# Optimization experiments

Measured on AMD Instinct MI355X. Metric: run time of the kernel, lower is better.

The kernel has to match this reference:

```python
import jax, jax.numpy as jnp
import numpy as np

N_NODES = 20000
N_EDGES = 256000
DIM = 128
N_LAYERS = 4


def _bn(x, gamma, beta, eps=1e-5):
    # BatchNorm1d in training mode: batch statistics over the node/edge axis
    mu = x.mean(0)
    var = ((x - mu) ** 2).mean(0)
    return gamma * (x - mu) * jax.lax.rsqrt(var + eps) + beta


def setup_inputs() -> dict:
    key = jax.random.key(0)
    ks = jax.random.split(key, 32)
    s = 1.0 / np.sqrt(DIM)
    inp = {
        'h': jax.random.normal(ks[0], (N_NODES, DIM), jnp.float32),
        'e': jax.random.normal(ks[1], (N_EDGES, DIM), jnp.float32),
        'src': jax.random.randint(ks[2], (N_EDGES,), 0, N_NODES, jnp.int32),
        'dst': jax.random.randint(ks[3], (N_EDGES,), 0, N_NODES, jnp.int32),
        'W_emb_h': jax.random.normal(ks[4], (DIM, DIM), jnp.float32) * s,
        'b_emb_h': jnp.zeros((DIM,), jnp.float32),
        'W_emb_e': jax.random.normal(ks[5], (DIM, DIM), jnp.float32) * s,
        'b_emb_e': jnp.zeros((DIM,), jnp.float32),
    }
    for i, nm in enumerate(['A', 'B', 'C', 'D', 'E']):
        inp[nm + 'w'] = jax.random.normal(ks[6 + i], (N_LAYERS, DIM, DIM), jnp.float32) * s
        inp[nm + 'b'] = jnp.zeros((N_LAYERS, DIM), jnp.float32)
    inp['gh'] = jnp.ones((N_LAYERS, DIM), jnp.float32)
    inp['bh'] = jnp.zeros((N_LAYERS, DIM), jnp.float32)
    inp['ge'] = jnp.ones((N_LAYERS, DIM), jnp.float32)
    inp['be'] = jnp.zeros((N_LAYERS, DIM), jnp.float32)
    return inp


def reference(h, e, src, dst, W_emb_h, b_emb_h, W_emb_e, b_emb_e,
              Aw, Ab, Bw, Bb, Cw, Cb, Dw, Db, Ew, Eb, gh, bh, ge, be):
    n_nodes = h.shape[0]
    # input embeddings
    h = h @ W_emb_h + b_emb_h
    e = e @ W_emb_e + b_emb_e
    for l in range(Aw.shape[0]):
        h_in, e_in = h, e
        Ah = h @ Aw[l] + Ab[l]
        Bh = h @ Bw[l] + Bb[l]
        Dh = h @ Dw[l] + Db[l]
        Eh = h @ Ew[l] + Eb[l]
        Ce = e @ Cw[l] + Cb[l]
        # edge gates: e_ij = D h_i + E h_j + C e_ij  (edge i->j)
        e_new = Dh[src] + Eh[dst] + Ce            # [E, D]
        sigma = jax.nn.sigmoid(e_new)
        num = jax.ops.segment_sum(sigma * Bh[src], dst, num_segments=n_nodes)
        den = jax.ops.segment_sum(sigma, dst, num_segments=n_nodes)
        h_new = Ah + num / (den + 1e-6)
        h_new = _bn(h_new, gh[l], bh[l])
        e_new = _bn(e_new, ge[l], be[l])
        # relu + residual (dropout = 0)
        h = h_in + jax.nn.relu(h_new)
        e = e_in + jax.nn.relu(e_new)
    return h
```

## Files before the change

kernel.cpp:

```cpp
#include <hip/hip_runtime.h>
#include <hip/hip_bf16.h>

typedef __attribute__((ext_vector_type(8))) short short8;
typedef __attribute__((ext_vector_type(4))) float floatx4;
typedef __attribute__((ext_vector_type(4))) unsigned short ushortx4;

typedef __attribute__((address_space(3))) unsigned int lds_u32;
typedef __attribute__((address_space(1))) const unsigned int g_u32;

__device__ __forceinline__ float bf2f(unsigned short u) {
    union { float f; unsigned int i; } v; v.i = ((unsigned int)u) << 16; return v.f;
}
__device__ __forceinline__ unsigned short f2bf(float f) {
    union { float f; unsigned int i; } v; v.f = f;
    unsigned int r = v.i + 0x7fffu + ((v.i >> 16) & 1u);
    return (unsigned short)(r >> 16);
}

__global__ void deg_count(const int* __restrict__ dst, int* __restrict__ deg, int E) {
    int i = blockIdx.x * 256 + threadIdx.x;
    if (i < E) atomicAdd(&deg[dst[i]], 1);
}

__global__ __launch_bounds__(1024) void scan_rowptr(const int* __restrict__ deg,
                                                    int* __restrict__ rowptr,
                                                    int* __restrict__ cursor, int N) {
    const int CH = 20;
    __shared__ int buf[1024];
    int t = threadIdx.x;
    int base = t * CH;
    int local[CH];
    int tot = 0;
#pragma unroll
    for (int k = 0; k < CH; ++k) {
        int i = base + k;
        int v = (i < N) ? deg[i] : 0;
        local[k] = tot;
        tot += v;
    }
    buf[t] = tot;
    __syncthreads();
    for (int off = 1; off < 1024; off <<= 1) {
        int x = (t >= off) ? buf[t - off] : 0;
        __syncthreads();
        buf[t] += x;
        __syncthreads();
    }
    int excl = buf[t] - tot;
#pragma unroll
    for (int k = 0; k < CH; ++k) {
        int i = base + k;
        if (i < N) { rowptr[i] = excl + local[k]; cursor[i] = excl + local[k]; }
    }
    if (t == 1023) rowptr[N] = buf[1023];
}

__global__ void scatter_edges(const int* __restrict__ src, const int* __restrict__ dst,
                              int* __restrict__ cursor, int* __restrict__ eix,
                              int* __restrict__ sx, int* __restrict__ dstx, int E) {
    int i = blockIdx.x * 256 + threadIdx.x;
    if (i >= E) return;
    int d = dst[i];
    int pos = atomicAdd(&cursor[d], 1);
    eix[pos] = i;
    sx[pos] = src[i];
    dstx[pos] = d;
}

__global__ void transpose_w(const float* __restrict__ Wh,
                            const float* __restrict__ We,
                            const float* __restrict__ Aw,
                            const float* __restrict__ Bw,
                            const float* __restrict__ Cw,
                            const float* __restrict__ Dw,
                            const float* __restrict__ Ew,
                            unsigned short* __restrict__ Wt) {
    int i = blockIdx.x * 256 + threadIdx.x;
    const int total = 22 * 16384;
    if (i >= total) return;
    int slot = i >> 14;
    int r = i & 16383;
    int n = r >> 7;
    int k = r & 127;
    const float* srcp;
    if (slot == 0) srcp = Wh;
    else if (slot == 1) srcp = We;
    else {
        int t = slot - 2;
        int l = t / 5, w = t % 5;
        const float* bases[5] = {Aw, Bw, Cw, Dw, Ew};
        srcp = bases[w] + l * 16384;
    }
    Wt[i] = f2bf(srcp[k * 128 + n]);
}

template <int IN_F32, int OUT_BF16, int GATHER>
__global__ __launch_bounds__(256) void gemm_lds(const void* __restrict__ Ain,
                                                const int* __restrict__ ridx,
                                                const unsigned short* __restrict__ Wt,
                                                const float* __restrict__ bias,
                                                void* __restrict__ Cout,
                                                int nTiles, int Mrows) {
    constexpr int ROWB = IN_F32 ? 512 : 256;
    constexpr int RSH = IN_F32 ? 9 : 8;
    constexpr int TILEB = 64 * ROWB;
    constexpr int PERW = TILEB / 4;
    constexpr int ROUNDS = PERW / 1024;
    __shared__ unsigned char smem[2][TILEB];

    const int lane = threadIdx.x & 63;
    const int wv = threadIdx.x >> 6;
    const int m16 = lane & 15;
    const int kg = lane >> 4;

    short8 b[4][2];
#pragma unroll
    for (int j = 0; j < 2; ++j)
#pragma unroll
        for (int ks = 0; ks < 4; ++ks)
            b[ks][j] = *(const short8*)(Wt + ((wv * 2 + j) * 16 + m16) * 128 + ks * 32 + kg * 8);
    floatx4 bv[2];
#pragma unroll
    for (int j = 0; j < 2; ++j)
        bv[j] = *(const floatx4*)(bias + (wv * 2 + j) * 16 + kg * 4);

    const unsigned char* Ab = (const unsigned char*)Ain;

    int t0 = blockIdx.x;
    if (t0 >= nTiles) return;

    auto stage = [&](int bufsel, int t) {
#pragma unroll
        for (int r = 0; r < ROUNDS; ++r) {
            int d = wv * PERW + r * 1024 + lane * 16;
            int row = d >> RSH;
            int scol;
            if (IN_F32)
                scol = (d ^ ((row & 3) << 5)) & (ROWB - 1);
            else
                scol = (d ^ ((row & 7) << 4)) & (ROWB - 1);
            int grow = t * 64 + row;
            grow = grow < Mrows ? grow : Mrows - 1;
            if (GATHER) grow = ridx[grow];
            const unsigned char* gp = Ab + (size_t)grow * ROWB + scol;
            unsigned char* lp = &smem[bufsel][wv * PERW + r * 1024];
            __builtin_amdgcn_global_load_lds((g_u32*)gp, (lds_u32*)lp, 16, 0, 0);
        }
    };

    int cur = 0;
    stage(0, t0);
    __syncthreads();

    for (int t = t0; t < nTiles; t += gridDim.x) {
        int tn = t + gridDim.x;
        if (tn < nTiles) stage(cur ^ 1, tn);

        const unsigned char* sb = smem[cur];
#pragma unroll
        for (int st = 0; st < 4; ++st) {
            short8 a[4];
#pragma unroll
            for (int ks = 0; ks < 4; ++ks) {
                if (IN_F32) {
                    int aoff = (st * 16 + m16) * 512 + ks * 128 + kg * 32;
                    aoff ^= (m16 & 3) << 5;
                    floatx4 f0 = *(const floatx4*)(sb + aoff);
                    floatx4 f1 = *(const floatx4*)(sb + aoff + 16);
                    short8 tt;
                    tt[0] = (short)f2bf(f0[0]); tt[1] = (short)f2bf(f0[1]);
                    tt[2] = (short)f2bf(f0[2]); tt[3] = (short)f2bf(f0[3]);
                    tt[4] = (short)f2bf(f1[0]); tt[5] = (short)f2bf(f1[1]);
                    tt[6] = (short)f2bf(f1[2]); tt[7] = (short)f2bf(f1[3]);
                    a[ks] = tt;
                } else {
                    int aoff = (st * 16 + m16) * 256 + ks * 64 + kg * 16;
                    aoff ^= (m16 & 7) << 4;
                    a[ks] = *(const short8*)(sb + aoff);
                }
            }
            floatx4 acc0 = (floatx4){0.f, 0.f, 0.f, 0.f};
            floatx4 acc1 = (floatx4){0.f, 0.f, 0.f, 0.f};
#pragma unroll
            for (int ks = 0; ks < 4; ++ks) {
                acc0 = __builtin_amdgcn_mfma_f32_16x16x32_bf16(b[ks][0], a[ks], acc0, 0, 0, 0);
                acc1 = __builtin_amdgcn_mfma_f32_16x16x32_bf16(b[ks][1], a[ks], acc1, 0, 0, 0);
            }
            size_t row = (size_t)t * 64 + st * 16 + m16;
#pragma unroll
            for (int j = 0; j < 2; ++j) {
                int c0 = (wv * 2 + j) * 16 + kg * 4;
                floatx4 accj = j ? acc1 : acc0;
                if (OUT_BF16) {
                    ushortx4 o;
#pragma unroll
                    for (int i = 0; i < 4; ++i) o[i] = f2bf(accj[i] + bv[j][i]);
                    *(ushortx4*)((unsigned short*)Cout + row * 128 + c0) = o;
                } else {
                    floatx4 o;
#pragma unroll
                    for (int i = 0; i < 4; ++i) o[i] = accj[i] + bv[j][i];
                    *(floatx4*)((float*)Cout + row * 128 + c0) = o;
                }
            }
        }
        __syncthreads();
        cur ^= 1;
    }
}

template <int STATS>
__global__ __launch_bounds__(256) void gemm_ce(const unsigned short* __restrict__ Ain,
                                               const unsigned short* __restrict__ Wt,
                                               const float* __restrict__ bias,
                                               const int* __restrict__ sx,
                                               const int* __restrict__ dstx,
                                               const unsigned short* __restrict__ Dh16,
                                               const unsigned short* __restrict__ Eh16,
                                               unsigned short* __restrict__ e_new,
                                               float* __restrict__ sums,
                                               int nTiles) {
    constexpr int TILEB = 64 * 256;
    constexpr int PERW = TILEB / 4;
    constexpr int ROUNDS = PERW / 1024;
    __shared__ unsigned char smem[2][TILEB];
    __shared__ float ls[256];

    const int lane = threadIdx.x & 63;
    const int wv = threadIdx.x >> 6;
    const int m16 = lane & 15;
    const int kg = lane >> 4;

    short8 b[4][2];
#pragma unroll
    for (int j = 0; j < 2; ++j)
#pragma unroll
        for (int ks = 0; ks < 4; ++ks)
            b[ks][j] = *(const short8*)(Wt + ((wv * 2 + j) * 16 + m16) * 128 + ks * 32 + kg * 8);
    floatx4 bv[2];
#pragma unroll
    for (int j = 0; j < 2; ++j)
        bv[j] = *(const floatx4*)(bias + (wv * 2 + j) * 16 + kg * 4);

    float es[2][4], eq[2][4];
#pragma unroll
    for (int j = 0; j < 2; ++j)
#pragma unroll
        for (int i = 0; i < 4; ++i) { es[j][i] = 0.f; eq[j][i] = 0.f; }

    const unsigned char* Ab = (const unsigned char*)Ain;

    int t0 = blockIdx.x;

    auto stage = [&](int bufsel, int t) {
#pragma unroll
        for (int r = 0; r < ROUNDS; ++r) {
            int d = wv * PERW + r * 1024 + lane * 16;
            int row = d >> 8;
            int scol = (d ^ ((row & 7) << 4)) & 255;
            const unsigned char* gp = Ab + (size_t)(t * 64 + row) * 256 + scol;
            unsigned char* lp = &smem[bufsel][wv * PERW + r * 1024];
            __builtin_amdgcn_global_load_lds((g_u32*)gp, (lds_u32*)lp, 16, 0, 0);
        }
    };

    int cur = 0;
    if (t0 < nTiles) {
        stage(0, t0);
        __syncthreads();

        for (int t = t0; t < nTiles; t += gridDim.x) {
            int tn = t + gridDim.x;
            if (tn < nTiles) stage(cur ^ 1, tn);

            const unsigned char* sb = smem[cur];
#pragma unroll
            for (int st = 0; st < 4; ++st) {
                int erow = t * 64 + st * 16 + m16;
                int sr = sx[erow];
                int dr = dstx[erow];
                short8 a[4];
#pragma unroll
                for (int ks = 0; ks < 4; ++ks) {
                    int aoff = (st * 16 + m16) * 256 + ks * 64 + kg * 16;
                    aoff ^= (m16 & 7) << 4;
                    a[ks] = *(const short8*)(sb + aoff);
                }
                floatx4 acc0 = (floatx4){0.f, 0.f, 0.f, 0.f};
                floatx4 acc1 = (floatx4){0.f, 0.f, 0.f, 0.f};
#pragma unroll
                for (int ks = 0; ks < 4; ++ks) {
                    acc0 = __builtin_amdgcn_mfma_f32_16x16x32_bf16(b[ks][0], a[ks], acc0, 0, 0, 0);
                    acc1 = __builtin_amdgcn_mfma_f32_16x16x32_bf16(b[ks][1], a[ks], acc1, 0, 0, 0);
                }
#pragma unroll
                for (int j = 0; j < 2; ++j) {
                    int c0 = (wv * 2 + j) * 16 + kg * 4;
                    floatx4 accj = j ? acc1 : acc0;
                    ushortx4 dh = *(const ushortx4*)(Dh16 + (size_t)sr * 128 + c0);
                    ushortx4 eh = *(const ushortx4*)(Eh16 + (size_t)dr * 128 + c0);
                    ushortx4 o;
#pragma unroll
                    for (int i = 0; i < 4; ++i) {
                        float en = accj[i] + bv[j][i] + bf2f(dh[i]) + bf2f(eh[i]);
                        o[i] = f2bf(en);
                        if (STATS) { es[j][i] += en; eq[j][i] += en * en; }
                    }
                    *(ushortx4*)(e_new + (size_t)erow * 128 + c0) = o;
                }
            }
            __syncthreads();
            cur ^= 1;
        }
    }

    if (STATS) {
        ls[threadIdx.x] = 0.f;
        __syncthreads();
#pragma unroll
        for (int j = 0; j < 2; ++j) {
            int c0 = (wv * 2 + j) * 16 + kg * 4;
#pragma unroll
            for (int i = 0; i < 4; ++i) {
                atomicAdd(&ls[c0 + i], es[j][i]);
                atomicAdd(&ls[(c0 + i) ^ 128], eq[j][i]);
            }
        }
        __syncthreads();
        atomicAdd(&sums[256 + threadIdx.x], ls[threadIdx.x]);
    }
}

__global__ __launch_bounds__(1024) void gemm_h4(const float* __restrict__ h_cur,
                                                const unsigned short* __restrict__ WtL,
                                                const float* __restrict__ Abi,
                                                const float* __restrict__ Bbi,
                                                const float* __restrict__ Dbi,
                                                const float* __restrict__ Ebi,
                                                float* __restrict__ AhB,
                                                unsigned short* __restrict__ Bh16,
                                                unsigned short* __restrict__ Dh16,
                                                unsigned short* __restrict__ Eh16,
                                                int nStrips) {
    const int lane = threadIdx.x & 63;
    const int w = threadIdx.x >> 6;
    const int grp = w >> 2;
    const int ntb = (w & 3) * 2;
    const int m16 = lane & 15;
    const int kg = lane >> 4;

    const int slotmap[4] = {0, 1, 3, 4};
    const float* biasmap[4] = {Abi, Bbi, Dbi, Ebi};
    const unsigned short* Wm = WtL + slotmap[grp] * 16384;
    const float* bp = biasmap[grp];

    short8 bf[4][2];
    floatx4 bv[2];
#pragma unroll
    for (int j = 0; j < 2; ++j) {
#pragma unroll
        for (int ks = 0; ks < 4; ++ks)
            bf[ks][j] = *(const short8*)(Wm + ((ntb + j) * 16 + m16) * 128 + ks * 32 + kg * 8);
        bv[j] = *(const floatx4*)(bp + (ntb + j) * 16 + kg * 4);
    }

    for (int s = blockIdx.x; s < nStrips; s += gridDim.x) {
        size_t rowBase = ((size_t)s * 16 + m16) * 128;
        short8 a[4];
#pragma unroll
        for (int ks = 0; ks < 4; ++ks) {
            int off = ks * 32 + kg * 8;
            floatx4 f0 = *(const floatx4*)(h_cur + rowBase + off);
            floatx4 f1 = *(const floatx4*)(h_cur + rowBase + off + 4);
            short8 t;
            t[0] = (short)f2bf(f0[0]); t[1] = (short)f2bf(f0[1]);
            t[2] = (short)f2bf(f0[2]); t[3] = (short)f2bf(f0[3]);
            t[4] = (short)f2bf(f1[0]); t[5] = (short)f2bf(f1[1]);
            t[6] = (short)f2bf(f1[2]); t[7] = (short)f2bf(f1[3]);
            a[ks] = t;
        }

        floatx4 acc0 = (floatx4){0.f, 0.f, 0.f, 0.f};
        floatx4 acc1 = (floatx4){0.f, 0.f, 0.f, 0.f};
#pragma unroll
        for (int ks = 0; ks < 4; ++ks) {
            acc0 = __builtin_amdgcn_mfma_f32_16x16x32_bf16(bf[ks][0], a[ks], acc0, 0, 0, 0);
            acc1 = __builtin_amdgcn_mfma_f32_16x16x32_bf16(bf[ks][1], a[ks], acc1, 0, 0, 0);
        }

        size_t r = (size_t)s * 16 + m16;
        if (grp == 0) {
            floatx4 o0, o1;
#pragma unroll
            for (int i = 0; i < 4; ++i) { o0[i] = acc0[i] + bv[0][i]; o1[i] = acc1[i] + bv[1][i]; }
            *(floatx4*)(AhB + r * 128 + (ntb + 0) * 16 + kg * 4) = o0;
            *(floatx4*)(AhB + r * 128 + (ntb + 1) * 16 + kg * 4) = o1;
        } else {
            unsigned short* outp = (grp == 1) ? Bh16 : (grp == 2) ? Dh16 : Eh16;
            ushortx4 o0, o1;
#pragma unroll
            for (int i = 0; i < 4; ++i) {
                o0[i] = f2bf(acc0[i] + bv[0][i]);
                o1[i] = f2bf(acc1[i] + bv[1][i]);
            }
            *(ushortx4*)(outp + r * 128 + (ntb + 0) * 16 + kg * 4) = o0;
            *(ushortx4*)(outp + r * 128 + (ntb + 1) * 16 + kg * 4) = o1;
        }
    }
}

__global__ __launch_bounds__(256) void node_aggregate(const unsigned short* __restrict__ e_new,
                                                      const unsigned short* __restrict__ Bh16,
                                                      const int* __restrict__ rowptr,
                                                      const int* __restrict__ sx,
                                                      const float* __restrict__ Ah,
                                                      float* __restrict__ h_new,
                                                      float* __restrict__ sums, int N) {
    const int q = threadIdx.x & 31;
    const int g = threadIdx.x >> 5;
    float hs[4] = {0.f, 0.f, 0.f, 0.f};
    float hq[4] = {0.f, 0.f, 0.f, 0.f};
    for (int d = blockIdx.x * 8 + g; d < N; d += gridDim.x * 8) {
        int beg = rowptr[d], end = rowptr[d + 1];
        float num[4] = {0.f, 0.f, 0.f, 0.f};
        float den[4] = {0.f, 0.f, 0.f, 0.f};
        int j = beg;
        for (; j + 3 < end; j += 4) {
            int s0 = sx[j], s1 = sx[j + 1], s2 = sx[j + 2], s3 = sx[j + 3];
            ushortx4 e0 = *(const ushortx4*)(e_new + (size_t)j * 128 + q * 4);
            ushortx4 e1 = *(const ushortx4*)(e_new + (size_t)(j + 1) * 128 + q * 4);
            ushortx4 e2 = *(const ushortx4*)(e_new + (size_t)(j + 2) * 128 + q * 4);
            ushortx4 e3 = *(const ushortx4*)(e_new + (size_t)(j + 3) * 128 + q * 4);
            ushortx4 b0 = *(const ushortx4*)(Bh16 + (size_t)s0 * 128 + q * 4);
            ushortx4 b1 = *(const ushortx4*)(Bh16 + (size_t)s1 * 128 + q * 4);
            ushortx4 b2 = *(const ushortx4*)(Bh16 + (size_t)s2 * 128 + q * 4);
            ushortx4 b3 = *(const ushortx4*)(Bh16 + (size_t)s3 * 128 + q * 4);
#pragma unroll
            for (int k = 0; k < 4; ++k) {
                float sg0 = __builtin_amdgcn_rcpf(1.f + __expf(-bf2f(e0[k])));
                float sg1 = __builtin_amdgcn_rcpf(1.f + __expf(-bf2f(e1[k])));
                float sg2 = __builtin_amdgcn_rcpf(1.f + __expf(-bf2f(e2[k])));
                float sg3 = __builtin_amdgcn_rcpf(1.f + __expf(-bf2f(e3[k])));
                den[k] += (sg0 + sg1) + (sg2 + sg3);
                num[k] += sg0 * bf2f(b0[k]) + sg1 * bf2f(b1[k])
                        + sg2 * bf2f(b2[k]) + sg3 * bf2f(b3[k]);
            }
        }
        for (; j < end; ++j) {
            int s0 = sx[j];
            ushortx4 e0 = *(const ushortx4*)(e_new + (size_t)j * 128 + q * 4);
            ushortx4 b0 = *(const ushortx4*)(Bh16 + (size_t)s0 * 128 + q * 4);
#pragma unroll
            for (int k = 0; k < 4; ++k) {
                float sg0 = __builtin_amdgcn_rcpf(1.f + __expf(-bf2f(e0[k])));
                den[k] += sg0;
                num[k] += sg0 * bf2f(b0[k]);
            }
        }
        floatx4 ah = *(const floatx4*)(Ah + (size_t)d * 128 + q * 4);
        floatx4 out;
#pragma unroll
        for (int k = 0; k < 4; ++k) {
            float v = ah[k] + num[k] / (den[k] + 1e-6f);
            out[k] = v;
            hs[k] += v;
            hq[k] += v * v;
        }
        *(floatx4*)(h_new + (size_t)d * 128 + q * 4) = out;
    }
    __shared__ float ls[256];
    ls[threadIdx.x] = 0.f;
    __syncthreads();
#pragma unroll
    for (int k = 0; k < 4; ++k) {
        atomicAdd(&ls[q * 4 + k], hs[k]);
        atomicAdd(&ls[128 + q * 4 + k], hq[k]);
    }
    __syncthreads();
    atomicAdd(&sums[threadIdx.x], ls[threadIdx.x]);
}

__global__ void finalize_stats(const float* __restrict__ sums,
                               const float* __restrict__ gh,
                               const float* __restrict__ bh,
                               const float* __restrict__ ge,
                               const float* __restrict__ be,
                               float* __restrict__ coef, int N, int E) {
    int c = threadIdx.x;
    if (c >= 128) return;
    float muh = sums[c] / (float)N;
    float vh = fmaxf(sums[128 + c] / (float)N - muh * muh, 0.f);
    float rsh = rsqrtf(vh + 1e-5f);
    float g = gh[c], bt = bh[c];
    coef[c] = g * rsh;
    coef[128 + c] = bt - g * rsh * muh;
    float mue = sums[256 + c] / (float)E;
    float ve = fmaxf(sums[384 + c] / (float)E - mue * mue, 0.f);
    float rse = rsqrtf(ve + 1e-5f);
    float g2 = ge[c], b2 = be[c];
    coef[256 + c] = g2 * rse;
    coef[384 + c] = b2 - g2 * rse * mue;
}

__global__ __launch_bounds__(256) void h_update(const float* __restrict__ h_new,
                                                const float* __restrict__ coef,
                                                float* __restrict__ h_cur,
                                                float* __restrict__ out, int N) {
    const int c = threadIdx.x & 127;
    float sa = coef[c], sb = coef[128 + c];
    int total = N * 128;
    for (int i = blockIdx.x * blockDim.x + threadIdx.x; i < total; i += gridDim.x * blockDim.x) {
        float v = h_new[i] * sa + sb;
        v = v > 0.f ? v : 0.f;
        float h = h_cur[i] + v;
        h_cur[i] = h;
        if (out) out[i] = h;
    }
}

__global__ __launch_bounds__(256) void e_update(const unsigned short* __restrict__ e_new,
                                                const float* __restrict__ coef,
                                                unsigned short* __restrict__ e_cur, int E) {
    int total8 = E * 16;
    for (int idx = blockIdx.x * blockDim.x + threadIdx.x; idx < total8;
         idx += gridDim.x * blockDim.x) {
        int c8 = (idx & 15) * 8;
        short8 en = *(const short8*)(e_new + (size_t)idx * 8);
        short8 ec = *(const short8*)(e_cur + (size_t)idx * 8);
        floatx4 sa0 = *(const floatx4*)(coef + 256 + c8);
        floatx4 sa1 = *(const floatx4*)(coef + 256 + c8 + 4);
        floatx4 sb0 = *(const floatx4*)(coef + 384 + c8);
        floatx4 sb1 = *(const floatx4*)(coef + 384 + c8 + 4);
        short8 r;
#pragma unroll
        for (int k = 0; k < 8; ++k) {
            float sa = (k < 4) ? sa0[k] : sa1[k - 4];
            float sb = (k < 4) ? sb0[k] : sb1[k - 4];
            float v = bf2f((unsigned short)en[k]) * sa + sb;
            v = v > 0.f ? v : 0.f;
            r[k] = (short)f2bf(bf2f((unsigned short)ec[k]) + v);
        }
        *(short8*)(e_cur + (size_t)idx * 8) = r;
    }
}

extern "C" void kernel_launch(void* const* d_in, const int* in_sizes, int n_in,
                              void* d_out, int out_size, void* d_ws, size_t ws_size,
                              hipStream_t stream) {
    const int N = 20000, E = 256000, L = 4;
    const int NPAD = 20032;

    const float* h_in = (const float*)d_in[0];
    const float* e_in = (const float*)d_in[1];
    const int* src = (const int*)d_in[2];
    const int* dst = (const int*)d_in[3];
    const float* Wemb_h = (const float*)d_in[4];
    const float* bemb_h = (const float*)d_in[5];
    const float* Wemb_e = (const float*)d_in[6];
    const float* bemb_e = (const float*)d_in[7];
    const float* Aw = (const float*)d_in[8];
    const float* Abi = (const float*)d_in[9];
    const float* Bw = (const float*)d_in[10];
    const float* Bbi = (const float*)d_in[11];
    const float* Cw = (const float*)d_in[12];
    const float* Cbi = (const float*)d_in[13];
    const float* Dw = (const float*)d_in[14];
    const float* Dbi = (const float*)d_in[15];
    const float* Ew = (const float*)d_in[16];
    const float* Ebi = (const float*)d_in[17];
    const float* gh = (const float*)d_in[18];
    const float* bh = (const float*)d_in[19];
    const float* ge = (const float*)d_in[20];
    const float* be = (const float*)d_in[21];

    char* p = (char*)d_ws;
    auto carve = [&](size_t bytes) {
        void* r = (void*)p;
        p += ((bytes + 255) & ~(size_t)255);
        return r;
    };
    unsigned short* Wt = (unsigned short*)carve((size_t)22 * 16384 * 2);
    float* h_cur = (float*)carve((size_t)NPAD * 128 * 4);
    unsigned short* e_cur = (unsigned short*)carve((size_t)E * 128 * 2);
    unsigned short* e_new = (unsigned short*)carve((size_t)E * 128 * 2);
    float* AhB = (float*)carve((size_t)N * 128 * 4);
    unsigned short* Bh16 = (unsigned short*)carve((size_t)N * 128 * 2);
    unsigned short* Dh16 = (unsigned short*)carve((size_t)N * 128 * 2);
    unsigned short* Eh16 = (unsigned short*)carve((size_t)N * 128 * 2);
    float* h_newB = (float*)carve((size_t)N * 128 * 4);
    float* sums = (float*)carve(4 * 128 * 4);
    float* coef = (float*)carve(4 * 128 * 4);
    int* deg = (int*)carve((size_t)N * 4);
    int* rowptr = (int*)carve((size_t)(N + 1) * 4);
    int* cursor = (int*)carve((size_t)N * 4);
    int* eix = (int*)carve((size_t)E * 4);
    int* sx = (int*)carve((size_t)E * 4);
    int* dstx = (int*)carve((size_t)E * 4);

    hipMemsetAsync(deg, 0, (size_t)N * 4, stream);
    deg_count<<<(E + 255) / 256, 256, 0, stream>>>(dst, deg, E);
    scan_rowptr<<<1, 1024, 0, stream>>>(deg, rowptr, cursor, N);
    scatter_edges<<<(E + 255) / 256, 256, 0, stream>>>(src, dst, cursor, eix, sx, dstx, E);

    transpose_w<<<(22 * 16384 + 255) / 256, 256, 0, stream>>>(Wemb_h, Wemb_e, Aw, Bw, Cw, Dw, Ew, Wt);

    gemm_lds<1, 0, 0><<<313, 256, 0, stream>>>(h_in, nullptr, Wt + 0 * 16384, bemb_h,
                                               h_cur, 313, N);
    gemm_lds<1, 1, 1><<<1024, 256, 0, stream>>>(e_in, eix, Wt + 1 * 16384, bemb_e,
                                                e_cur, E / 64, E);

    for (int l = 0; l < L; ++l) {
        int last = (l == L - 1);
        hipMemsetAsync(sums, 0, 4 * 128 * 4, stream);
        const unsigned short* WtL = Wt + (size_t)(2 + l * 5) * 16384;
        gemm_h4<<<250, 1024, 0, stream>>>(h_cur, WtL, Abi + l * 128, Bbi + l * 128,
                                          Dbi + l * 128, Ebi + l * 128, AhB, Bh16, Dh16, Eh16,
                                          N / 16);
        if (!last)
            gemm_ce<1><<<1024, 256, 0, stream>>>(e_cur, WtL + 2 * 16384, Cbi + l * 128,
                                                 sx, dstx, Dh16, Eh16, e_new, sums, E / 64);
        else
            gemm_ce<0><<<1024, 256, 0, stream>>>(e_cur, WtL + 2 * 16384, Cbi + l * 128,
                                                 sx, dstx, Dh16, Eh16, e_new, sums, E / 64);
        node_aggregate<<<1250, 256, 0, stream>>>(e_new, Bh16, rowptr, sx, AhB,
                                                 h_newB, sums, N);
        finalize_stats<<<1, 128, 0, stream>>>(sums, gh + l * 128, bh + l * 128, ge + l * 128,
                                              be + l * 128, coef, N, E);
        h_update<<<512, 256, 0, stream>>>(h_newB, coef, h_cur, last ? (float*)d_out : nullptr, N);
        if (!last) e_update<<<2048, 256, 0, stream>>>(e_new, coef, e_cur, E);
    }
}
```

Measured before the change: 1.046 ms.

## Fuse sigmoid-gated scatter aggregation into edge GEMM with segmented atomics

Computes the sigmoid gate and sigma*Bh products inside the edge GEMM epilogue. Runs of equal destinations within each 16-row strip are pre-reduced with a shuffle scan, and the sums go to per-node num/den buffers via global float atomics. The separate CSR aggregation pass, and in the last layer the e_new store, are removed; a light node_combine kernel does the division and stats. In exchange it adds a large per-layer memset, many global atomics (edges are dst-sorted, so runs shorten them), and nondeterministic summation order.

Measured after the change: 1.477 ms. 41.2% more time.

```diff
diff --git a/kernel.cpp b/kernel.cpp
--- a/kernel.cpp
+++ b/kernel.cpp
@@ -215,9 +215,12 @@
                                                const float* __restrict__ bias,
                                                const int* __restrict__ sx,
                                                const int* __restrict__ dstx,
+                                               const unsigned short* __restrict__ Bh16,
                                                const unsigned short* __restrict__ Dh16,
                                                const unsigned short* __restrict__ Eh16,
                                                unsigned short* __restrict__ e_new,
+                                               float* __restrict__ num,
+                                               float* __restrict__ den,
                                                float* __restrict__ sums,
                                                int nTiles) {
     constexpr int TILEB = 64 * 256;
@@ -273,12 +276,27 @@
             int tn = t + gridDim.x;
             if (tn < nTiles) stage(cur ^ 1, tn);
 
-            const unsigned char* sb = smem[cur];
+            int sxv[4], dxv[4];
 #pragma unroll
             for (int st = 0; st < 4; ++st) {
                 int erow = t * 64 + st * 16 + m16;
-                int sr = sx[erow];
-                int dr = dstx[erow];
+                sxv[st] = sx[erow];
+                dxv[st] = dstx[erow];
+            }
+
+            const unsigned char* sb = smem[cur];
+#pragma unroll
+            for (int st = 0; st < 4; ++st) {
+                int erow = t * 64 + st * 16 + m16;
+                int sr = sxv[st], dr = dxv[st];
+                ushortx4 dh[2], eh[2], bh[2];
+#pragma unroll
+                for (int j = 0; j < 2; ++j) {
+                    int c0 = (wv * 2 + j) * 16 + kg * 4;
+                    dh[j] = *(const ushortx4*)(Dh16 + (size_t)sr * 128 + c0);
+                    eh[j] = *(const ushortx4*)(Eh16 + (size_t)dr * 128 + c0);
+                    bh[j] = *(const ushortx4*)(Bh16 + (size_t)sr * 128 + c0);
+                }
                 short8 a[4];
 #pragma unroll
                 for (int ks = 0; ks < 4; ++ks) {
@@ -293,20 +311,48 @@
                     acc0 = __builtin_amdgcn_mfma_f32_16x16x32_bf16(b[ks][0], a[ks], acc0, 0, 0, 0);
                     acc1 = __builtin_amdgcn_mfma_f32_16x16x32_bf16(b[ks][1], a[ks], acc1, 0, 0, 0);
                 }
+                float nm[2][4], dn[2][4];
 #pragma unroll
                 for (int j = 0; j < 2; ++j) {
                     int c0 = (wv * 2 + j) * 16 + kg * 4;
                     floatx4 accj = j ? acc1 : acc0;
-                    ushortx4 dh = *(const ushortx4*)(Dh16 + (size_t)sr * 128 + c0);
-                    ushortx4 eh = *(const ushortx4*)(Eh16 + (size_t)dr * 128 + c0);
                     ushortx4 o;
 #pragma unroll
                     for (int i = 0; i < 4; ++i) {
-                        float en = accj[i] + bv[j][i] + bf2f(dh[i]) + bf2f(eh[i]);
-                        o[i] = f2bf(en);
-                        if (STATS) { es[j][i] += en; eq[j][i] += en * en; }
+                        float en = accj[i] + bv[j][i] + bf2f(dh[j][i]) + bf2f(eh[j][i]);
+                        if (STATS) { es[j][i] += en; eq[j][i] += en * en; o[i] = f2bf(en); }
+                        float sg = __builtin_amdgcn_rcpf(1.f + __expf(-en));
+                        dn[j][i] = sg;
+                        nm[j][i] = sg * bf2f(bh[j][i]);
                     }
-                    *(ushortx4*)(e_new + (size_t)erow * 128 + c0) = o;
+                    if (STATS) *(ushortx4*)(e_new + (size_t)erow * 128 + c0) = o;
+                }
+                int myd = dr;
+#pragma unroll
+                for (int off = 1; off < 16; off <<= 1) {
+                    int od = __shfl_up(myd, off, 16);
+                    bool take = (m16 >= off) && (od == myd);
+#pragma unroll
+                    for (int j = 0; j < 2; ++j)
+#pragma unroll
+                        for (int i = 0; i < 4; ++i) {
+                            float nv = __shfl_up(nm[j][i], off, 16);
+                            float dv = __shfl_up(dn[j][i], off, 16);
+                            if (take) { nm[j][i] += nv; dn[j][i] += dv; }
+                        }
+                }
+                int nd = __shfl_down(myd, 1, 16);
+                bool tail = (m16 == 15) || (nd != myd);
+                if (tail) {
+#pragma unroll
+                    for (int j = 0; j < 2; ++j) {
+                        int c0 = (wv * 2 + j) * 16 + kg * 4;
+#pragma unroll
+                        for (int i = 0; i < 4; ++i) {
+                            atomicAdd(&num[(size_t)myd * 128 + c0 + i], nm[j][i]);
+                            atomicAdd(&den[(size_t)myd * 128 + c0 + i], dn[j][i]);
+                        }
+                    }
                 }
             }
             __syncthreads();
@@ -323,7 +369,7 @@
 #pragma unroll
             for (int i = 0; i < 4; ++i) {
                 atomicAdd(&ls[c0 + i], es[j][i]);
-                atomicAdd(&ls[(c0 + i) ^ 128], eq[j][i]);
+                atomicAdd(&ls[128 + c0 + i], eq[j][i]);
             }
         }
         __syncthreads();
@@ -409,59 +455,23 @@
     }
 }
 
-__global__ __launch_bounds__(256) void node_aggregate(const unsigned short* __restrict__ e_new,
-                                                      const unsigned short* __restrict__ Bh16,
-                                                      const int* __restrict__ rowptr,
-                                                      const int* __restrict__ sx,
-                                                      const float* __restrict__ Ah,
-                                                      float* __restrict__ h_new,
-                                                      float* __restrict__ sums, int N) {
+__global__ __launch_bounds__(256) void node_combine(const float* __restrict__ Ah,
+                                                    const float* __restrict__ num,
+                                                    const float* __restrict__ den,
+                                                    float* __restrict__ h_new,
+                                                    float* __restrict__ sums, int N) {
     const int q = threadIdx.x & 31;
     const int g = threadIdx.x >> 5;
     float hs[4] = {0.f, 0.f, 0.f, 0.f};
     float hq[4] = {0.f, 0.f, 0.f, 0.f};
     for (int d = blockIdx.x * 8 + g; d < N; d += gridDim.x * 8) {
-        int beg = rowptr[d], end = rowptr[d + 1];
-        float num[4] = {0.f, 0.f, 0.f, 0.f};
-        float den[4] = {0.f, 0.f, 0.f, 0.f};
-        int j = beg;
-        for (; j + 3 < end; j += 4) {
-            int s0 = sx[j], s1 = sx[j + 1], s2 = sx[j + 2], s3 = sx[j + 3];
-            ushortx4 e0 = *(const ushortx4*)(e_new + (size_t)j * 128 + q * 4);
-            ushortx4 e1 = *(const ushortx4*)(e_new + (size_t)(j + 1) * 128 + q * 4);
-            ushortx4 e2 = *(const ushortx4*)(e_new + (size_t)(j + 2) * 128 + q * 4);
-            ushortx4 e3 = *(const ushortx4*)(e_new + (size_t)(j + 3) * 128 + q * 4);
-            ushortx4 b0 = *(const ushortx4*)(Bh16 + (size_t)s0 * 128 + q * 4);
-            ushortx4 b1 = *(const ushortx4*)(Bh16 + (size_t)s1 * 128 + q * 4);
-            ushortx4 b2 = *(const ushortx4*)(Bh16 + (size_t)s2 * 128 + q * 4);
-            ushortx4 b3 = *(const ushortx4*)(Bh16 + (size_t)s3 * 128 + q * 4);
-#pragma unroll
-            for (int k = 0; k < 4; ++k) {
-                float sg0 = __builtin_amdgcn_rcpf(1.f + __expf(-bf2f(e0[k])));
-                float sg1 = __builtin_amdgcn_rcpf(1.f + __expf(-bf2f(e1[k])));
-                float sg2 = __builtin_amdgcn_rcpf(1.f + __expf(-bf2f(e2[k])));
-                float sg3 = __builtin_amdgcn_rcpf(1.f + __expf(-bf2f(e3[k])));
-                den[k] += (sg0 + sg1) + (sg2 + sg3);
-                num[k] += sg0 * bf2f(b0[k]) + sg1 * bf2f(b1[k])
-                        + sg2 * bf2f(b2[k]) + sg3 * bf2f(b3[k]);
-            }
-        }
-        for (; j < end; ++j) {
-            int s0 = sx[j];
-            ushortx4 e0 = *(const ushortx4*)(e_new + (size_t)j * 128 + q * 4);
-            ushortx4 b0 = *(const ushortx4*)(Bh16 + (size_t)s0 * 128 + q * 4);
-#pragma unroll
-            for (int k = 0; k < 4; ++k) {
-                float sg0 = __builtin_amdgcn_rcpf(1.f + __expf(-bf2f(e0[k])));
-                den[k] += sg0;
-                num[k] += sg0 * bf2f(b0[k]);
-            }
-        }
         floatx4 ah = *(const floatx4*)(Ah + (size_t)d * 128 + q * 4);
+        floatx4 nm = *(const floatx4*)(num + (size_t)d * 128 + q * 4);
+        floatx4 dn = *(const floatx4*)(den + (size_t)d * 128 + q * 4);
         floatx4 out;
 #pragma unroll
         for (int k = 0; k < 4; ++k) {
-            float v = ah[k] + num[k] / (den[k] + 1e-6f);
+            float v = ah[k] + nm[k] / (dn[k] + 1e-6f);
             out[k] = v;
             hs[k] += v;
             hq[k] += v * v;
@@ -588,6 +598,7 @@
     unsigned short* Dh16 = (unsigned short*)carve((size_t)N * 128 * 2);
     unsigned short* Eh16 = (unsigned short*)carve((size_t)N * 128 * 2);
     float* h_newB = (float*)carve((size_t)N * 128 * 4);
+    float* numden = (float*)carve((size_t)N * 128 * 4 * 2);
     float* sums = (float*)carve(4 * 128 * 4);
     float* coef = (float*)carve(4 * 128 * 4);
     int* deg = (int*)carve((size_t)N * 4);
@@ -596,6 +607,8 @@
     int* eix = (int*)carve((size_t)E * 4);
     int* sx = (int*)carve((size_t)E * 4);
     int* dstx = (int*)carve((size_t)E * 4);
+    float* num = numden;
+    float* den = numden + (size_t)N * 128;
 
     hipMemsetAsync(deg, 0, (size_t)N * 4, stream);
     deg_count<<<(E + 255) / 256, 256, 0, stream>>>(dst, deg, E);
@@ -612,18 +625,20 @@
     for (int l = 0; l < L; ++l) {
         int last = (l == L - 1);
         hipMemsetAsync(sums, 0, 4 * 128 * 4, stream);
+        hipMemsetAsync(numden, 0, (size_t)N * 128 * 4 * 2, stream);
         const unsigned short* WtL = Wt + (size_t)(2 + l * 5) * 16384;
         gemm_h4<<<250, 1024, 0, stream>>>(h_cur, WtL, Abi + l * 128, Bbi + l * 128,
                                           Dbi + l * 128, Ebi + l * 128, AhB, Bh16, Dh16, Eh16,
                                           N / 16);
         if (!last)
             gemm_ce<1><<<1024, 256, 0, stream>>>(e_cur, WtL + 2 * 16384, Cbi + l * 128,
-                                                 sx, dstx, Dh16, Eh16, e_new, sums, E / 64);
+                                                 sx, dstx, Bh16, Dh16, Eh16, e_new,
+                                                 num, den, sums, E / 64);
         else
             gemm_ce<0><<<1024, 256, 0, stream>>>(e_cur, WtL + 2 * 16384, Cbi + l * 128,
-                                                 sx, dstx, Dh16, Eh16, e_new, sums, E / 64);
-        node_aggregate<<<1250, 256, 0, stream>>>(e_new, Bh16, rowptr, sx, AhB,
-                                                 h_newB, sums, N);
+                                                 sx, dstx, Bh16, Dh16, Eh16, e_new,
+                                                 num, den, sums, E / 64);
+        node_combine<<<2500, 256, 0, stream>>>(AhB, num, den, h_newB, sums, N);
         finalize_stats<<<1, 128, 0, stream>>>(sums, gh + l * 128, bh + l * 128, ge + l * 128,
                                               be + l * 128, coef, N, E);
         h_update<<<512, 256, 0, stream>>>(h_newB, coef, h_cur, last ? (float*)d_out : nullptr, N);
```
